# Optimization experiments

Hardware: AMD Instinct MI355X
Metric: run time of the kernel (lower is better)

## Reference

```python
import jax, jax.numpy as jnp
import numpy as np

N, E = 100000, 1280000
IN_D, FEAT, HID, OUT = 256, 64, 64, 64
NEG_SLOPE = 0.2


def _gat_conv(x, src, dst, w, a_s, a_d, b, n):
    # x: [N, in], w: [in, out], a_s/a_d/b: [out]; edges src->dst (messages flow to dst)
    h = x @ w                                   # [N, out]
    e = jax.nn.leaky_relu((h @ a_s)[src] + (h @ a_d)[dst], NEG_SLOPE)  # [E]
    m = jax.ops.segment_max(e, dst, num_segments=n)                     # scatter-softmax (stable)
    ex = jnp.exp(e - m[dst])
    den = jax.ops.segment_sum(ex, dst, num_segments=n)
    alpha = ex / (den[dst] + 1e-16)
    out = jax.ops.segment_sum(alpha[:, None] * h[src], dst, num_segments=n)
    return out + b


def setup_inputs() -> dict:
    key = jax.random.key(0)
    ks = jax.random.split(key, 16)
    rn = lambda k, shape, s=0.05: jax.random.normal(k, shape, jnp.float32) * s
    return {
        'x': jax.random.normal(ks[0], (N, IN_D), jnp.float32),
        'src': jax.random.randint(ks[1], (E,), 0, N),
        'dst': jax.random.randint(ks[2], (E,), 0, N),
        'lin_w': rn(ks[3], (IN_D, FEAT)), 'lin_b': jnp.zeros((FEAT,), jnp.float32),
        'w1': rn(ks[4], (FEAT, HID)), 'a1s': rn(ks[5], (HID,)), 'a1d': rn(ks[6], (HID,)), 'b1': jnp.zeros((HID,), jnp.float32),
        'w2': rn(ks[7], (HID, HID)), 'a2s': rn(ks[8], (HID,)), 'a2d': rn(ks[9], (HID,)), 'b2': jnp.zeros((HID,), jnp.float32),
        'w3': rn(ks[10], (HID, OUT)), 'a3s': rn(ks[11], (OUT,)), 'a3d': rn(ks[12], (OUT,)), 'b3': jnp.zeros((OUT,), jnp.float32),
    }


def reference(x, src, dst, lin_w, lin_b, w1, a1s, a1d, b1, w2, a2s, a2d, b2, w3, a3s, a3d, b3):
    n = x.shape[0]
    loop = jnp.arange(n, dtype=src.dtype)        # GATConv add_self_loops=True
    s = jnp.concatenate([src, loop])
    d = jnp.concatenate([dst, loop])
    h = x @ lin_w + lin_b                        # feature_pre linear
    h = jax.nn.relu(_gat_conv(h, s, d, w1, a1s, a1d, b1, n))  # dropout is identity in eval
    h = jax.nn.relu(_gat_conv(h, s, d, w2, a2s, a2d, b2, n))
    h = _gat_conv(h, s, d, w3, a3s, a3d, b3, n)
    norm = jnp.linalg.norm(h, axis=-1, keepdims=True)          # F.normalize(p=2, dim=-1)
    return h / jnp.maximum(norm, 1e-12)
```

## Files before the change

kernel.cpp:

```cpp
#include <hip/hip_runtime.h>


constexpr float NEG_SLOPE = 0.2f;
#define BKT_SHIFT 9
#define BKT_N     512
#define PCHUNK    2048
#define SRC_BITS  17

typedef __attribute__((ext_vector_type(8))) short bf16x8;
typedef __attribute__((ext_vector_type(4))) float f32x4;

__device__ inline ushort f2bf(float x) {
    union { float f; uint u; } v; v.f = x;
    return (ushort)((v.u + 0x7FFFu + ((v.u >> 16) & 1u)) >> 16);
}
__device__ inline void bf2f(uint u, float& lo, float& hi) {
    union { uint u; float f; } a, b;
    a.u = u << 16; b.u = u & 0xFFFF0000u;
    lo = a.f; hi = b.f;
}
__device__ inline uint pk(float a, float b) {
    return (uint)f2bf(a) | ((uint)f2bf(b) << 16);
}

__global__ __launch_bounds__(256) void prep_w(
    const float* __restrict__ lw, const float* __restrict__ w1,
    const float* __restrict__ w2, const float* __restrict__ w3,
    ushort* __restrict__ lwT, ushort* __restrict__ w1T,
    ushort* __restrict__ w2T, ushort* __restrict__ w3T,
    int* __restrict__ cnt, int* __restrict__ ticket, int n)
{
    const int i = blockIdx.x * 256 + threadIdx.x;
    if (i < n) cnt[i] = 0;
    if (i == 0) *ticket = 0;
    if (i < 64 * 256) {
        const int nn = i >> 8, k = i & 255;
        lwT[i] = f2bf(lw[k * 64 + nn]);
    } else {
        const int j = i - 64 * 256;
        if (j < 4096) {
            const int nn = j >> 6, k = j & 63;
            w1T[j] = f2bf(w1[k * 64 + nn]);
            w2T[j] = f2bf(w2[k * 64 + nn]);
            w3T[j] = f2bf(w3[k * 64 + nn]);
        }
    }
}

__device__ __forceinline__ void gemm_pre_tile(
    const float* __restrict__ x, const ushort* __restrict__ lwT,
    const float* __restrict__ bias, ushort* __restrict__ C, int M, int tile)
{
    __shared__ __align__(16) ushort ctile[4][16][64];
    const int tid = threadIdx.x;
    const int w = tid >> 6, lane = tid & 63;
    const int rw0 = (tile * 4 + w) * 16;
    if (rw0 >= M) return;
    const int c = lane & 15, q = lane >> 4;

    const float* ap = x + (size_t)(rw0 + c) * 256 + q * 8;
    float4 pv[16];
    #pragma unroll
    for (int s = 0; s < 8; ++s) {
        pv[2 * s]     = *(const float4*)(ap + s * 32);
        pv[2 * s + 1] = *(const float4*)(ap + s * 32 + 4);
    }

    f32x4 acc[4];
    #pragma unroll
    for (int t = 0; t < 4; ++t) acc[t] = (f32x4){0.f, 0.f, 0.f, 0.f};

    #pragma unroll
    for (int s = 0; s < 8; ++s) {
        const float4 p0 = pv[2 * s];
        const float4 p1 = pv[2 * s + 1];
        bf16x8 af;
        af[0] = (short)f2bf(p0.x); af[1] = (short)f2bf(p0.y);
        af[2] = (short)f2bf(p0.z); af[3] = (short)f2bf(p0.w);
        af[4] = (short)f2bf(p1.x); af[5] = (short)f2bf(p1.y);
        af[6] = (short)f2bf(p1.z); af[7] = (short)f2bf(p1.w);
        #pragma unroll
        for (int t = 0; t < 4; ++t) {
            const bf16x8 bf = *(const bf16x8*)(lwT + (size_t)(t * 16 + c) * 256 + s * 32 + q * 8);
            acc[t] = __builtin_amdgcn_mfma_f32_16x16x32_bf16(af, bf, acc[t], 0, 0, 0);
        }
    }

    #pragma unroll
    for (int t = 0; t < 4; ++t) {
        const float bv = bias[t * 16 + c];
        #pragma unroll
        for (int r = 0; r < 4; ++r)
            ctile[w][q * 4 + r][t * 16 + c] = f2bf(acc[t][r] + bv);
    }
    const int row = lane >> 2, eo = (lane & 3) * 16;
    const uint4 v0 = *(const uint4*)(&ctile[w][row][eo]);
    const uint4 v1 = *(const uint4*)(&ctile[w][row][eo + 8]);
    *(uint4*)(C + (size_t)(rw0 + row) * 64 + eo)     = v0;
    *(uint4*)(C + (size_t)(rw0 + row) * 64 + eo + 8) = v1;
}

__global__ __launch_bounds__(256) void gemm_layer(
    const ushort* __restrict__ A, const ushort* __restrict__ WT,
    const float* __restrict__ a_s, const float* __restrict__ a_d,
    ushort* __restrict__ C, float* __restrict__ hs, float* __restrict__ hd, int M)
{
    __shared__ __align__(16) ushort ctile[4][16][64];
    const int tid = threadIdx.x;
    const int w = tid >> 6, lane = tid & 63;
    const int rw0 = (blockIdx.x * 4 + w) * 16;
    if (rw0 >= M) return;
    const int c = lane & 15, q = lane >> 4;

    const ushort* ap = A + (size_t)(rw0 + c) * 64 + q * 8;
    const bf16x8 a0 = *(const bf16x8*)(ap);
    const bf16x8 a1 = *(const bf16x8*)(ap + 32);

    f32x4 acc[4];
    #pragma unroll
    for (int t = 0; t < 4; ++t) {
        const ushort* bp = WT + (size_t)(t * 16 + c) * 64 + q * 8;
        const bf16x8 b0 = *(const bf16x8*)(bp);
        const bf16x8 b1 = *(const bf16x8*)(bp + 32);
        f32x4 a = (f32x4){0.f, 0.f, 0.f, 0.f};
        a = __builtin_amdgcn_mfma_f32_16x16x32_bf16(a0, b0, a, 0, 0, 0);
        a = __builtin_amdgcn_mfma_f32_16x16x32_bf16(a1, b1, a, 0, 0, 0);
        acc[t] = a;
    }

    float ps[4] = {0.f, 0.f, 0.f, 0.f}, pd[4] = {0.f, 0.f, 0.f, 0.f};
    #pragma unroll
    for (int t = 0; t < 4; ++t) {
        const float as = a_s[t * 16 + c], ad = a_d[t * 16 + c];
        #pragma unroll
        for (int r = 0; r < 4; ++r) {
            ps[r] = fmaf(acc[t][r], as, ps[r]);
            pd[r] = fmaf(acc[t][r], ad, pd[r]);
        }
    }
    #pragma unroll
    for (int r = 0; r < 4; ++r) {
        #pragma unroll
        for (int off = 1; off < 16; off <<= 1) {
            ps[r] += __shfl_xor(ps[r], off);
            pd[r] += __shfl_xor(pd[r], off);
        }
    }
    if (c == 0) {
        #pragma unroll
        for (int r = 0; r < 4; ++r) {
            hs[rw0 + q * 4 + r] = ps[r];
            hd[rw0 + q * 4 + r] = pd[r];
        }
    }

    #pragma unroll
    for (int t = 0; t < 4; ++t)
        #pragma unroll
        for (int r = 0; r < 4; ++r)
            ctile[w][q * 4 + r][t * 16 + c] = f2bf(acc[t][r]);
    const int row = lane >> 2, eo = (lane & 3) * 16;
    const uint4 v0 = *(const uint4*)(&ctile[w][row][eo]);
    const uint4 v1 = *(const uint4*)(&ctile[w][row][eo + 8]);
    *(uint4*)(C + (size_t)(rw0 + row) * 64 + eo)     = v0;
    *(uint4*)(C + (size_t)(rw0 + row) * 64 + eo + 8) = v1;
}

__global__ __launch_bounds__(256) void edge_hist(
    const int* __restrict__ dst, int* __restrict__ cnt, int e)
{
    const int i0 = (blockIdx.x * 256 + threadIdx.x) * 4;
    if (i0 + 3 < e) {
        const int4 d = *(const int4*)(dst + i0);
        atomicAdd(&cnt[d.x], 1); atomicAdd(&cnt[d.y], 1);
        atomicAdd(&cnt[d.z], 1); atomicAdd(&cnt[d.w], 1);
    } else {
        for (int k = i0; k < e; ++k) atomicAdd(&cnt[dst[k]], 1);
    }
}

__global__ __launch_bounds__(256) void scan1_tiles(
    const int* __restrict__ cnt, int* __restrict__ out,
    int* __restrict__ bsum, int* __restrict__ ticket, int n, int nblk,
    const float* __restrict__ x, const ushort* __restrict__ lwT,
    const float* __restrict__ lin_b, ushort* __restrict__ C, int M, int tile0)
{
    __shared__ int wsum[4];
    __shared__ int amLastS;
    if ((int)blockIdx.x >= nblk) {
        gemm_pre_tile(x, lwT, lin_b, C, M, tile0 + (int)blockIdx.x - nblk);
        return;
    }
    const int tid  = threadIdx.x;
    const int lane = tid & 63;
    const int w    = tid >> 6;
    const int base = blockIdx.x * 1024;
    int vals[4];
    int tsum = 0;
    #pragma unroll
    for (int i = 0; i < 4; ++i) {
        const int idx = base + tid * 4 + i;
        vals[i] = (idx < n) ? cnt[idx] : 0;
        tsum += vals[i];
    }
    int x1 = tsum;
    #pragma unroll
    for (int off = 1; off < 64; off <<= 1) {
        const int y = __shfl_up(x1, off);
        if (lane >= off) x1 += y;
    }
    if (lane == 63) wsum[w] = x1;
    __syncthreads();
    int wofs = 0;
    for (int k = 0; k < w; ++k) wofs += wsum[k];
    int excl = wofs + x1 - tsum;
    #pragma unroll
    for (int i = 0; i < 4; ++i) {
        const int idx = base + tid * 4 + i;
        if (idx < n) out[idx] = excl;
        excl += vals[i];
    }
    if (tid == 255) {
        bsum[blockIdx.x] = wofs + x1;
        __threadfence();
        amLastS = (atomicAdd(ticket, 1) == nblk - 1) ? 1 : 0;
    }
    __syncthreads();
    if (amLastS) {
        __threadfence();
        const int v2 = (tid < nblk) ? bsum[tid] : 0;
        int x2 = v2;
        #pragma unroll
        for (int off = 1; off < 64; off <<= 1) {
            const int y = __shfl_up(x2, off);
            if (lane >= off) x2 += y;
        }
        if (lane == 63) wsum[w] = x2;
        __syncthreads();
        int c2 = 0;
        for (int k = 0; k < w; ++k) c2 += wsum[k];
        if (tid < nblk) bsum[tid] = c2 + x2 - v2;
    }
}

__global__ __launch_bounds__(256) void scan3_tiles(
    int* __restrict__ out, const int* __restrict__ bsum,
    int* __restrict__ gcur, int n, int total, int s3b,
    const float* __restrict__ x, const ushort* __restrict__ lwT,
    const float* __restrict__ lin_b, ushort* __restrict__ C, int M, int tile0)
{
    if ((int)blockIdx.x >= s3b) {
        gemm_pre_tile(x, lwT, lin_b, C, M, tile0 + (int)blockIdx.x - s3b);
        return;
    }
    const int idx = blockIdx.x * 256 + threadIdx.x;
    if (idx < n) {
        const int v = out[idx] + bsum[idx >> 10];
        out[idx] = v;
        if ((idx & (BKT_N - 1)) == 0) gcur[idx >> BKT_SHIFT] = v;
    }
    if (idx == 0) out[n] = total;
}

__global__ __launch_bounds__(256) void part_tiles(
    const int* __restrict__ src, const int* __restrict__ dst,
    int* __restrict__ gcursor, int* __restrict__ pairs, int e, int nb, int pb,
    const float* __restrict__ x, const ushort* __restrict__ lwT,
    const float* __restrict__ lin_b, ushort* __restrict__ C, int M, int tile0)
{
    __shared__ int stage[PCHUNK];
    __shared__ unsigned char sbkt[PCHUNK];
    __shared__ int lcnt[256];
    __shared__ int lstart[256];
    __shared__ int lfill[256];
    __shared__ int gbase[256];
    __shared__ int wsum[4];

    if ((int)blockIdx.x >= pb) {
        gemm_pre_tile(x, lwT, lin_b, C, M, tile0 + (int)blockIdx.x - pb);
        return;
    }

    const int tid  = threadIdx.x;
    const int lane = tid & 63;
    const int w    = tid >> 6;
    const int base = blockIdx.x * PCHUNK;
    const int cnt_here = min(PCHUNK, e - base);

    lcnt[tid] = 0; lfill[tid] = 0;
    __syncthreads();

    for (int i = tid; i < cnt_here; i += 256)
        atomicAdd(&lcnt[dst[base + i] >> BKT_SHIFT], 1);
    __syncthreads();

    const int v = lcnt[tid];
    int x1 = v;
    #pragma unroll
    for (int off = 1; off < 64; off <<= 1) {
        const int y = __shfl_up(x1, off);
        if (lane >= off) x1 += y;
    }
    if (lane == 63) wsum[w] = x1;
    __syncthreads();
    int carry = 0;
    for (int k = 0; k < w; ++k) carry += wsum[k];
    lstart[tid] = carry + x1 - v;
    if (tid < nb && v > 0) gbase[tid] = atomicAdd(&gcursor[tid], v);
    __syncthreads();

    for (int i = tid; i < cnt_here; i += 256) {
        const int d = dst[base + i];
        const int s = src[base + i];
        const int b = d >> BKT_SHIFT;
        const int p = lstart[b] + atomicAdd(&lfill[b], 1);
        stage[p] = ((d & (BKT_N - 1)) << SRC_BITS) | s;
        sbkt[p]  = (unsigned char)b;
    }
    __syncthreads();

    for (int t = tid; t < cnt_here; t += 256) {
        const int b = sbkt[t];
        pairs[gbase[b] + (t - lstart[b])] = stage[t];
    }
}

__global__ __launch_bounds__(256) void scat_tiles(
    const int* __restrict__ pairs, const int* __restrict__ offs,
    int* __restrict__ ssrc, int n, int sb,
    const float* __restrict__ x, const ushort* __restrict__ lwT,
    const float* __restrict__ lin_b, ushort* __restrict__ C, int M, int tile0)
{
    __shared__ int pos[BKT_N];
    if ((int)blockIdx.x >= sb) {
        gemm_pre_tile(x, lwT, lin_b, C, M, tile0 + (int)blockIdx.x - sb);
        return;
    }
    const int node0 = blockIdx.x << BKT_SHIFT;
    const int node1 = min(n, node0 + BKT_N);
    const int tid = threadIdx.x;
    for (int i = tid; i < node1 - node0; i += 256) pos[i] = offs[node0 + i];
    __syncthreads();
    const int e0 = offs[node0];
    const int e1 = offs[node1];
    for (int j = e0 + tid; j < e1; j += 256) {
        const int pr = pairs[j];
        const int p = atomicAdd(&pos[pr >> SRC_BITS], 1);
        ssrc[p] = pr & ((1 << SRC_BITS) - 1);
    }
}

template <int MODE>
__global__ __launch_bounds__(256) void gat_agg(
    const ushort* __restrict__ hp, const float* __restrict__ hs,
    const float* __restrict__ hd, const int* __restrict__ offs,
    const int* __restrict__ ssrc, const float* __restrict__ bias,
    void* __restrict__ outv, int n)
{
    const int wid  = (blockIdx.x * blockDim.x + threadIdx.x) >> 6;
    const int lane = threadIdx.x & 63;
    if (wid >= n) return;
    const int sub = lane >> 3;
    const int f0  = (lane & 7) * 8;

    const int start = offs[wid];
    const int end   = offs[wid + 1];
    const float hdi = hd[wid];

    int j = start + sub;
    bool vC = j < end;
    bool vN = j + 8 < end;
    int sC = vC ? ssrc[j]     : wid;
    int sN = vN ? ssrc[j + 8] : sC;

    float den = 0.f;
    float acc[8] = {};

    if (sub == 0) {
        const uint4 t = *(const uint4*)(hp + (size_t)wid * 64 + f0);
        float e = hs[wid] + hdi;
        e = (e > 0.f) ? e : NEG_SLOPE * e;
        const float ex = __expf(e);
        float f[8];
        bf2f(t.x, f[0], f[1]); bf2f(t.y, f[2], f[3]);
        bf2f(t.z, f[4], f[5]); bf2f(t.w, f[6], f[7]);
        den = ex;
        #pragma unroll
        for (int i = 0; i < 8; ++i) acc[i] = ex * f[i];
    }

    float hsC = hs[sC];
    uint4 tC  = *(const uint4*)(hp + (size_t)sC * 64 + f0);

    while (vC) {
        const bool vNN = j + 16 < end;
        const int  sNN = vNN ? ssrc[j + 16] : sN;
        const float hsN = hs[sN];
        const uint4 tN  = *(const uint4*)(hp + (size_t)sN * 64 + f0);

        float e2 = hsC + hdi;
        e2 = (e2 > 0.f) ? e2 : NEG_SLOPE * e2;
        const float ex2 = __expf(e2);
        float f[8];
        bf2f(tC.x, f[0], f[1]); bf2f(tC.y, f[2], f[3]);
        bf2f(tC.z, f[4], f[5]); bf2f(tC.w, f[6], f[7]);
        den += ex2;
        #pragma unroll
        for (int i = 0; i < 8; ++i) acc[i] = fmaf(ex2, f[i], acc[i]);

        vC = vN; vN = vNN; sC = sN; sN = sNN; hsC = hsN; tC = tN;
        j += 8;
    }

    #pragma unroll
    for (int off = 8; off < 64; off <<= 1) {
        den += __shfl_xor(den, off);
        #pragma unroll
        for (int i = 0; i < 8; ++i) acc[i] += __shfl_xor(acc[i], off);
    }

    const float4 bv0 = *(const float4*)(bias + f0);
    const float4 bv1 = *(const float4*)(bias + f0 + 4);
    const float bb[8] = {bv0.x, bv0.y, bv0.z, bv0.w, bv1.x, bv1.y, bv1.z, bv1.w};
    const float inv = 1.f / (den + 1e-16f);
    float v[8];
    #pragma unroll
    for (int i = 0; i < 8; ++i) v[i] = acc[i] * inv + bb[i];

    if (MODE == 0) {
        #pragma unroll
        for (int i = 0; i < 8; ++i) v[i] = fmaxf(v[i], 0.f);
        if (sub == 0) {
            uint4 o;
            o.x = pk(v[0], v[1]); o.y = pk(v[2], v[3]);
            o.z = pk(v[4], v[5]); o.w = pk(v[6], v[7]);
            *(uint4*)((ushort*)outv + (size_t)wid * 64 + f0) = o;
        }
    } else {
        float sq = 0.f;
        #pragma unroll
        for (int i = 0; i < 8; ++i) sq += v[i] * v[i];
        #pragma unroll
        for (int off = 1; off < 8; off <<= 1) sq += __shfl_xor(sq, off);
        const float s = 1.f / fmaxf(sqrtf(sq), 1e-12f);
        if (sub == 0) {
            float* op = (float*)outv + (size_t)wid * 64 + f0;
            float4 o0, o1;
            o0.x = v[0] * s; o0.y = v[1] * s; o0.z = v[2] * s; o0.w = v[3] * s;
            o1.x = v[4] * s; o1.y = v[5] * s; o1.z = v[6] * s; o1.w = v[7] * s;
            *(float4*)(op)     = o0;
            *(float4*)(op + 4) = o1;
        }
    }
}

extern "C" void kernel_launch(void* const* d_in, const int* in_sizes, int n_in,
                              void* d_out, int out_size, void* d_ws, size_t ws_size,
                              hipStream_t stream)
{
    const float* x     = (const float*)d_in[0];
    const int*   src   = (const int*)d_in[1];
    const int*   dst   = (const int*)d_in[2];
    const float* lin_w = (const float*)d_in[3];
    const float* lin_b = (const float*)d_in[4];
    const float* w1  = (const float*)d_in[5];
    const float* a1s = (const float*)d_in[6];
    const float* a1d = (const float*)d_in[7];
    const float* b1  = (const float*)d_in[8];
    const float* w2  = (const float*)d_in[9];
    const float* a2s = (const float*)d_in[10];
    const float* a2d = (const float*)d_in[11];
    const float* b2  = (const float*)d_in[12];
    const float* w3  = (const float*)d_in[13];
    const float* a3s = (const float*)d_in[14];
    const float* a3d = (const float*)d_in[15];
    const float* b3  = (const float*)d_in[16];

    const int n = in_sizes[0] / 256;
    const int E = in_sizes[1];
    const int nb = (n + BKT_N - 1) >> BKT_SHIFT;

    char* wsp = (char*)d_ws;
    auto alloc = [&](size_t bytes) -> void* {
        void* p = (void*)wsp;
        wsp += (bytes + 255) & ~(size_t)255;
        return p;
    };
    ushort* bufA = (ushort*)alloc((size_t)n * 64 * sizeof(ushort));
    ushort* bufB = (ushort*)alloc((size_t)n * 64 * sizeof(ushort));
    float*  hs   = (float*)alloc((size_t)n * sizeof(float));
    float*  hd   = (float*)alloc((size_t)n * sizeof(float));
    int*    offs = (int*)alloc((size_t)(n + 1) * sizeof(int));
    int*    cnt  = (int*)alloc((size_t)n * sizeof(int));
    int*    bsum = (int*)alloc(1024 * sizeof(int));
    int*    gcur = (int*)alloc(256 * sizeof(int));
    int*    tick = (int*)alloc(256 * sizeof(int));
    int*    ssrc = (int*)alloc((size_t)E * sizeof(int));
    int*    pairs = (int*)alloc((size_t)E * sizeof(int));
    ushort* lwT = (ushort*)alloc(64 * 256 * sizeof(ushort));
    ushort* w1T = (ushort*)alloc(64 * 64 * sizeof(ushort));
    ushort* w2T = (ushort*)alloc(64 * 64 * sizeof(ushort));
    ushort* w3T = (ushort*)alloc(64 * 64 * sizeof(ushort));

    const int nodeWaveBlocks = (n + 3) / 4;
    const int gemmBlocks = (n + 63) / 64;
    const int nScanBlocks = (n + 1023) / 1024;
    const int s3Blocks = (n + 255) / 256;
    const int histBlocks = (E / 4 + 255) / 256 + 1;
    const int partBlocks = (E + PCHUNK - 1) / PCHUNK;

    const int TA = 200;
    const int TB = 300;
    const int TC = 400;
    const int TD = gemmBlocks - TA - TB - TC;

    prep_w<<<(n + 255) / 256, 256, 0, stream>>>(
        lin_w, w1, w2, w3, lwT, w1T, w2T, w3T, cnt, tick, n);
    edge_hist<<<histBlocks, 256, 0, stream>>>(dst, cnt, E);
    scan1_tiles<<<nScanBlocks + TA, 256, 0, stream>>>(
        cnt, offs, bsum, tick, n, nScanBlocks,
        x, lwT, lin_b, bufA, n, 0);
    scan3_tiles<<<s3Blocks + TB, 256, 0, stream>>>(
        offs, bsum, gcur, n, E, s3Blocks,
        x, lwT, lin_b, bufA, n, TA);
    part_tiles<<<partBlocks + TC, 256, 0, stream>>>(
        src, dst, gcur, pairs, E, nb, partBlocks,
        x, lwT, lin_b, bufA, n, TA + TB);
    scat_tiles<<<nb + TD, 256, 0, stream>>>(
        pairs, offs, ssrc, n, nb,
        x, lwT, lin_b, bufA, n, TA + TB + TC);

    gemm_layer<<<gemmBlocks, 256, 0, stream>>>(bufA, w1T, a1s, a1d, bufB, hs, hd, n);
    gat_agg<0><<<nodeWaveBlocks, 256, 0, stream>>>(bufB, hs, hd, offs, ssrc, b1, bufA, n);

    gemm_layer<<<gemmBlocks, 256, 0, stream>>>(bufA, w2T, a2s, a2d, bufB, hs, hd, n);
    gat_agg<0><<<nodeWaveBlocks, 256, 0, stream>>>(bufB, hs, hd, offs, ssrc, b2, bufA, n);

    gemm_layer<<<gemmBlocks, 256, 0, stream>>>(bufA, w3T, a3s, a3d, bufB, hs, hd, n);
    gat_agg<1><<<nodeWaveBlocks, 256, 0, stream>>>(bufB, hs, hd, offs, ssrc, b3,
                                                   d_out, n);
}
```

Measured before the change: 497.0 us.

## Fuse layer GEMMs into pre-linear and aggregation kernels with precomputed attention vectors

Fuses the first GAT layer's weight GEMM and attention projections into the pre-linear tile kernel by staging the bf16 result in LDS. It also fuses layers two and three's GEMMs into the preceding aggregation kernel via a new fused_ag kernel, and computes hs/hd from the aggregated row using precomputed W·a vectors. This removes three separate gemm_layer launches and their round trip of node features through global memory. In exchange, fused_ag processes 16 nodes per block with a serial 4-node loop per wave and two barriers, which lowers aggregation parallelism. The attention logits are now computed from the bf16-rounded input times an fp32 W·a rather than from the bf16 GEMM output, so they change slightly.

```diff
diff --git a/kernel.cpp b/kernel.cpp
--- a/kernel.cpp
+++ b/kernel.cpp
@@ -23,11 +23,20 @@
     return (uint)f2bf(a) | ((uint)f2bf(b) << 16);
 }
 
+struct PreArgs {
+    const float* x; const ushort* lwT; const float* lin_b;
+    const ushort* w1T; const float* a1s; const float* a1d;
+    ushort* C; float* hs; float* hd; int M;
+};
+
 __global__ __launch_bounds__(256) void prep_w(
     const float* __restrict__ lw, const float* __restrict__ w1,
     const float* __restrict__ w2, const float* __restrict__ w3,
+    const float* __restrict__ a2s, const float* __restrict__ a2d,
+    const float* __restrict__ a3s, const float* __restrict__ a3d,
     ushort* __restrict__ lwT, ushort* __restrict__ w1T,
     ushort* __restrict__ w2T, ushort* __restrict__ w3T,
+    float* __restrict__ wvec,
     int* __restrict__ cnt, int* __restrict__ ticket, int n)
 {
     const int i = blockIdx.x * 256 + threadIdx.x;
@@ -36,40 +45,44 @@
     if (i < 64 * 256) {
         const int nn = i >> 8, k = i & 255;
         lwT[i] = f2bf(lw[k * 64 + nn]);
-    } else {
+    } else if (i < 64 * 256 + 4096) {
         const int j = i - 64 * 256;
-        if (j < 4096) {
-            const int nn = j >> 6, k = j & 63;
-            w1T[j] = f2bf(w1[k * 64 + nn]);
-            w2T[j] = f2bf(w2[k * 64 + nn]);
-            w3T[j] = f2bf(w3[k * 64 + nn]);
-        }
-    }
-}
-
-__device__ __forceinline__ void gemm_pre_tile(
-    const float* __restrict__ x, const ushort* __restrict__ lwT,
-    const float* __restrict__ bias, ushort* __restrict__ C, int M, int tile)
-{
+        const int nn = j >> 6, k = j & 63;
+        w1T[j] = f2bf(w1[k * 64 + nn]);
+        w2T[j] = f2bf(w2[k * 64 + nn]);
+        w3T[j] = f2bf(w3[k * 64 + nn]);
+    } else if (i < 64 * 256 + 4096 + 256) {
+        const int j = i - 64 * 256 - 4096;
+        const int p = j >> 6, k = j & 63;
+        const float* Wp = (p < 2) ? w2 : w3;
+        const float* vp = (p == 0) ? a2s : (p == 1) ? a2d : (p == 2) ? a3s : a3d;
+        float s = 0.f;
+        #pragma unroll
+        for (int t = 0; t < 64; ++t) s += Wp[k * 64 + t] * vp[t];
+        wvec[p * 64 + k] = s;
+    }
+}
+
+__device__ __forceinline__ void gemm_pre_fused(const PreArgs& pa, int tile)
+{
+    __shared__ __align__(16) ushort ldsA[4][8][16][8];
     __shared__ __align__(16) ushort ctile[4][16][64];
     const int tid = threadIdx.x;
     const int w = tid >> 6, lane = tid & 63;
     const int rw0 = (tile * 4 + w) * 16;
-    if (rw0 >= M) return;
+    if (rw0 >= pa.M) return;
     const int c = lane & 15, q = lane >> 4;
 
-    const float* ap = x + (size_t)(rw0 + c) * 256 + q * 8;
+    const float* ap = pa.x + (size_t)(rw0 + c) * 256 + q * 8;
     float4 pv[16];
     #pragma unroll
     for (int s = 0; s < 8; ++s) {
         pv[2 * s]     = *(const float4*)(ap + s * 32);
         pv[2 * s + 1] = *(const float4*)(ap + s * 32 + 4);
     }
-
     f32x4 acc[4];
     #pragma unroll
     for (int t = 0; t < 4; ++t) acc[t] = (f32x4){0.f, 0.f, 0.f, 0.f};
-
     #pragma unroll
     for (int s = 0; s < 8; ++s) {
         const float4 p0 = pv[2 * s];
@@ -81,61 +94,41 @@
         af[6] = (short)f2bf(p1.z); af[7] = (short)f2bf(p1.w);
         #pragma unroll
         for (int t = 0; t < 4; ++t) {
-            const bf16x8 bf = *(const bf16x8*)(lwT + (size_t)(t * 16 + c) * 256 + s * 32 + q * 8);
+            const bf16x8 bf = *(const bf16x8*)(pa.lwT + (size_t)(t * 16 + c) * 256 + s * 32 + q * 8);
             acc[t] = __builtin_amdgcn_mfma_f32_16x16x32_bf16(af, bf, acc[t], 0, 0, 0);
         }
     }
-
     #pragma unroll
     for (int t = 0; t < 4; ++t) {
-        const float bv = bias[t * 16 + c];
+        const float bv = pa.lin_b[t * 16 + c];
+        const int kb = 2 * t + (c >> 3);
+        const int e  = c & 7;
         #pragma unroll
         for (int r = 0; r < 4; ++r)
-            ctile[w][q * 4 + r][t * 16 + c] = f2bf(acc[t][r] + bv);
-    }
-    const int row = lane >> 2, eo = (lane & 3) * 16;
-    const uint4 v0 = *(const uint4*)(&ctile[w][row][eo]);
-    const uint4 v1 = *(const uint4*)(&ctile[w][row][eo + 8]);
-    *(uint4*)(C + (size_t)(rw0 + row) * 64 + eo)     = v0;
-    *(uint4*)(C + (size_t)(rw0 + row) * 64 + eo + 8) = v1;
-}
-
-__global__ __launch_bounds__(256) void gemm_layer(
-    const ushort* __restrict__ A, const ushort* __restrict__ WT,
-    const float* __restrict__ a_s, const float* __restrict__ a_d,
-    ushort* __restrict__ C, float* __restrict__ hs, float* __restrict__ hd, int M)
-{
-    __shared__ __align__(16) ushort ctile[4][16][64];
-    const int tid = threadIdx.x;
-    const int w = tid >> 6, lane = tid & 63;
-    const int rw0 = (blockIdx.x * 4 + w) * 16;
-    if (rw0 >= M) return;
-    const int c = lane & 15, q = lane >> 4;
-
-    const ushort* ap = A + (size_t)(rw0 + c) * 64 + q * 8;
-    const bf16x8 a0 = *(const bf16x8*)(ap);
-    const bf16x8 a1 = *(const bf16x8*)(ap + 32);
-
-    f32x4 acc[4];
+            ldsA[w][kb][q * 4 + r][e] = f2bf(acc[t][r] + bv);
+    }
+
+    const bf16x8 a0 = *(const bf16x8*)&ldsA[w][q][c][0];
+    const bf16x8 a1 = *(const bf16x8*)&ldsA[w][q + 4][c][0];
+    f32x4 acc2[4];
     #pragma unroll
     for (int t = 0; t < 4; ++t) {
-        const ushort* bp = WT + (size_t)(t * 16 + c) * 64 + q * 8;
+        const ushort* bp = pa.w1T + (size_t)(t * 16 + c) * 64 + q * 8;
         const bf16x8 b0 = *(const bf16x8*)(bp);
         const bf16x8 b1 = *(const bf16x8*)(bp + 32);
         f32x4 a = (f32x4){0.f, 0.f, 0.f, 0.f};
         a = __builtin_amdgcn_mfma_f32_16x16x32_bf16(a0, b0, a, 0, 0, 0);
         a = __builtin_amdgcn_mfma_f32_16x16x32_bf16(a1, b1, a, 0, 0, 0);
-        acc[t] = a;
-    }
-
+        acc2[t] = a;
+    }
     float ps[4] = {0.f, 0.f, 0.f, 0.f}, pd[4] = {0.f, 0.f, 0.f, 0.f};
     #pragma unroll
     for (int t = 0; t < 4; ++t) {
-        const float as = a_s[t * 16 + c], ad = a_d[t * 16 + c];
+        const float as = pa.a1s[t * 16 + c], ad = pa.a1d[t * 16 + c];
         #pragma unroll
         for (int r = 0; r < 4; ++r) {
-            ps[r] = fmaf(acc[t][r], as, ps[r]);
-            pd[r] = fmaf(acc[t][r], ad, pd[r]);
+            ps[r] = fmaf(acc2[t][r], as, ps[r]);
+            pd[r] = fmaf(acc2[t][r], ad, pd[r]);
         }
     }
     #pragma unroll
@@ -149,21 +142,20 @@
     if (c == 0) {
         #pragma unroll
         for (int r = 0; r < 4; ++r) {
-            hs[rw0 + q * 4 + r] = ps[r];
-            hd[rw0 + q * 4 + r] = pd[r];
+            pa.hs[rw0 + q * 4 + r] = ps[r];
+            pa.hd[rw0 + q * 4 + r] = pd[r];
         }
     }
-
     #pragma unroll
     for (int t = 0; t < 4; ++t)
         #pragma unroll
         for (int r = 0; r < 4; ++r)
-            ctile[w][q * 4 + r][t * 16 + c] = f2bf(acc[t][r]);
+            ctile[w][q * 4 + r][t * 16 + c] = f2bf(acc2[t][r]);
     const int row = lane >> 2, eo = (lane & 3) * 16;
     const uint4 v0 = *(const uint4*)(&ctile[w][row][eo]);
     const uint4 v1 = *(const uint4*)(&ctile[w][row][eo + 8]);
-    *(uint4*)(C + (size_t)(rw0 + row) * 64 + eo)     = v0;
-    *(uint4*)(C + (size_t)(rw0 + row) * 64 + eo + 8) = v1;
+    *(uint4*)(pa.C + (size_t)(rw0 + row) * 64 + eo)     = v0;
+    *(uint4*)(pa.C + (size_t)(rw0 + row) * 64 + eo + 8) = v1;
 }
 
 __global__ __launch_bounds__(256) void edge_hist(
@@ -182,13 +174,12 @@
 __global__ __launch_bounds__(256) void scan1_tiles(
     const int* __restrict__ cnt, int* __restrict__ out,
     int* __restrict__ bsum, int* __restrict__ ticket, int n, int nblk,
-    const float* __restrict__ x, const ushort* __restrict__ lwT,
-    const float* __restrict__ lin_b, ushort* __restrict__ C, int M, int tile0)
+    PreArgs pa, int tile0)
 {
     __shared__ int wsum[4];
     __shared__ int amLastS;
     if ((int)blockIdx.x >= nblk) {
-        gemm_pre_tile(x, lwT, lin_b, C, M, tile0 + (int)blockIdx.x - nblk);
+        gemm_pre_fused(pa, tile0 + (int)blockIdx.x - nblk);
         return;
     }
     const int tid  = threadIdx.x;
@@ -246,11 +237,10 @@
 __global__ __launch_bounds__(256) void scan3_tiles(
     int* __restrict__ out, const int* __restrict__ bsum,
     int* __restrict__ gcur, int n, int total, int s3b,
-    const float* __restrict__ x, const ushort* __restrict__ lwT,
-    const float* __restrict__ lin_b, ushort* __restrict__ C, int M, int tile0)
+    PreArgs pa, int tile0)
 {
     if ((int)blockIdx.x >= s3b) {
-        gemm_pre_tile(x, lwT, lin_b, C, M, tile0 + (int)blockIdx.x - s3b);
+        gemm_pre_fused(pa, tile0 + (int)blockIdx.x - s3b);
         return;
     }
     const int idx = blockIdx.x * 256 + threadIdx.x;
@@ -265,8 +255,7 @@
 __global__ __launch_bounds__(256) void part_tiles(
     const int* __restrict__ src, const int* __restrict__ dst,
     int* __restrict__ gcursor, int* __restrict__ pairs, int e, int nb, int pb,
-    const float* __restrict__ x, const ushort* __restrict__ lwT,
-    const float* __restrict__ lin_b, ushort* __restrict__ C, int M, int tile0)
+    PreArgs pa, int tile0)
 {
     __shared__ int stage[PCHUNK];
     __shared__ unsigned char sbkt[PCHUNK];
@@ -277,7 +266,7 @@
     __shared__ int wsum[4];
 
     if ((int)blockIdx.x >= pb) {
-        gemm_pre_tile(x, lwT, lin_b, C, M, tile0 + (int)blockIdx.x - pb);
+        gemm_pre_fused(pa, tile0 + (int)blockIdx.x - pb);
         return;
     }
 
@@ -328,12 +317,11 @@
 __global__ __launch_bounds__(256) void scat_tiles(
     const int* __restrict__ pairs, const int* __restrict__ offs,
     int* __restrict__ ssrc, int n, int sb,
-    const float* __restrict__ x, const ushort* __restrict__ lwT,
-    const float* __restrict__ lin_b, ushort* __restrict__ C, int M, int tile0)
+    PreArgs pa, int tile0)
 {
     __shared__ int pos[BKT_N];
     if ((int)blockIdx.x >= sb) {
-        gemm_pre_tile(x, lwT, lin_b, C, M, tile0 + (int)blockIdx.x - sb);
+        gemm_pre_fused(pa, tile0 + (int)blockIdx.x - sb);
         return;
     }
     const int node0 = blockIdx.x << BKT_SHIFT;
@@ -350,12 +338,147 @@
     }
 }
 
-template <int MODE>
-__global__ __launch_bounds__(256) void gat_agg(
+__global__ __launch_bounds__(256) void fused_ag(
+    const ushort* __restrict__ hp, const float* __restrict__ hsIn,
+    const float* __restrict__ hdIn, const int* __restrict__ offs,
+    const int* __restrict__ ssrc, const float* __restrict__ bias,
+    const ushort* __restrict__ WT, const float* __restrict__ waS,
+    const float* __restrict__ waD,
+    ushort* __restrict__ C, float* __restrict__ hsOut, float* __restrict__ hdOut,
+    int n)
+{
+    __shared__ __align__(16) ushort ldsA[8][16][8];
+    __shared__ __align__(16) ushort ldsC[16][68];
+    const int tid  = threadIdx.x;
+    const int w    = tid >> 6, lane = tid & 63;
+    const int rw0  = blockIdx.x * 16;
+    const int sub  = lane >> 3;
+    const int f0   = (lane & 7) * 8;
+
+    const float4 bv0 = *(const float4*)(bias + f0);
+    const float4 bv1 = *(const float4*)(bias + f0 + 4);
+    const float bb[8] = {bv0.x, bv0.y, bv0.z, bv0.w, bv1.x, bv1.y, bv1.z, bv1.w};
+    float ws8[8], wd8[8];
+    {
+        const float4 s0 = *(const float4*)(waS + f0);
+        const float4 s1 = *(const float4*)(waS + f0 + 4);
+        const float4 d0 = *(const float4*)(waD + f0);
+        const float4 d1 = *(const float4*)(waD + f0 + 4);
+        ws8[0]=s0.x; ws8[1]=s0.y; ws8[2]=s0.z; ws8[3]=s0.w;
+        ws8[4]=s1.x; ws8[5]=s1.y; ws8[6]=s1.z; ws8[7]=s1.w;
+        wd8[0]=d0.x; wd8[1]=d0.y; wd8[2]=d0.z; wd8[3]=d0.w;
+        wd8[4]=d1.x; wd8[5]=d1.y; wd8[6]=d1.z; wd8[7]=d1.w;
+    }
+
+    #pragma unroll 1
+    for (int i = 0; i < 4; ++i) {
+        const int rowIdx = w * 4 + i;
+        const int node = rw0 + rowIdx;
+        if (node < n) {
+            const int start = offs[node];
+            const int end   = offs[node + 1];
+            const float hdi = hdIn[node];
+
+            int j = start + sub;
+            bool vC = j < end;
+            bool vN = j + 8 < end;
+            int sC = vC ? ssrc[j]     : node;
+            int sN = vN ? ssrc[j + 8] : sC;
+
+            float den = 0.f;
+            float acc[8] = {};
+            if (sub == 0) {
+                const uint4 t = *(const uint4*)(hp + (size_t)node * 64 + f0);
+                float e = hsIn[node] + hdi;
+                e = (e > 0.f) ? e : NEG_SLOPE * e;
+                const float ex = __expf(e);
+                float f[8];
+                bf2f(t.x, f[0], f[1]); bf2f(t.y, f[2], f[3]);
+                bf2f(t.z, f[4], f[5]); bf2f(t.w, f[6], f[7]);
+                den = ex;
+                #pragma unroll
+                for (int k = 0; k < 8; ++k) acc[k] = ex * f[k];
+            }
+            float hsC = hsIn[sC];
+            uint4 tC  = *(const uint4*)(hp + (size_t)sC * 64 + f0);
+            while (vC) {
+                const bool vNN = j + 16 < end;
+                const int  sNN = vNN ? ssrc[j + 16] : sN;
+                const float hsN = hsIn[sN];
+                const uint4 tN  = *(const uint4*)(hp + (size_t)sN * 64 + f0);
+                float e2 = hsC + hdi;
+                e2 = (e2 > 0.f) ? e2 : NEG_SLOPE * e2;
+                const float ex2 = __expf(e2);
+                float f[8];
+                bf2f(tC.x, f[0], f[1]); bf2f(tC.y, f[2], f[3]);
+                bf2f(tC.z, f[4], f[5]); bf2f(tC.w, f[6], f[7]);
+                den += ex2;
+                #pragma unroll
+                for (int k = 0; k < 8; ++k) acc[k] = fmaf(ex2, f[k], acc[k]);
+                vC = vN; vN = vNN; sC = sN; sN = sNN; hsC = hsN; tC = tN;
+                j += 8;
+            }
+            #pragma unroll
+            for (int off = 8; off < 64; off <<= 1) {
+                den += __shfl_xor(den, off);
+                #pragma unroll
+                for (int k = 0; k < 8; ++k) acc[k] += __shfl_xor(acc[k], off);
+            }
+            const float inv = 1.f / (den + 1e-16f);
+            float v[8];
+            #pragma unroll
+            for (int k = 0; k < 8; ++k)
+                v[k] = fmaxf(acc[k] * inv + bb[k], 0.f);
+            uint4 o;
+            o.x = pk(v[0], v[1]); o.y = pk(v[2], v[3]);
+            o.z = pk(v[4], v[5]); o.w = pk(v[6], v[7]);
+            float rv[8];
+            bf2f(o.x, rv[0], rv[1]); bf2f(o.y, rv[2], rv[3]);
+            bf2f(o.z, rv[4], rv[5]); bf2f(o.w, rv[6], rv[7]);
+            float psum = 0.f, pdum = 0.f;
+            #pragma unroll
+            for (int k = 0; k < 8; ++k) {
+                psum = fmaf(rv[k], ws8[k], psum);
+                pdum = fmaf(rv[k], wd8[k], pdum);
+            }
+            #pragma unroll
+            for (int off = 1; off < 8; off <<= 1) {
+                psum += __shfl_xor(psum, off);
+                pdum += __shfl_xor(pdum, off);
+            }
+            if (lane == 0) { hsOut[node] = psum; hdOut[node] = pdum; }
+            if (sub == 0) *(uint4*)&ldsA[lane & 7][rowIdx][0] = o;
+        } else if (sub == 0) {
+            const uint4 z = {0u, 0u, 0u, 0u};
+            *(uint4*)&ldsA[lane & 7][rowIdx][0] = z;
+        }
+    }
+    __syncthreads();
+
+    const int c = lane & 15, q = lane >> 4;
+    const bf16x8 a0 = *(const bf16x8*)&ldsA[q][c][0];
+    const bf16x8 a1 = *(const bf16x8*)&ldsA[q + 4][c][0];
+    const ushort* bp = WT + (size_t)(w * 16 + c) * 64 + q * 8;
+    const bf16x8 b0 = *(const bf16x8*)(bp);
+    const bf16x8 b1 = *(const bf16x8*)(bp + 32);
+    f32x4 a = (f32x4){0.f, 0.f, 0.f, 0.f};
+    a = __builtin_amdgcn_mfma_f32_16x16x32_bf16(a0, b0, a, 0, 0, 0);
+    a = __builtin_amdgcn_mfma_f32_16x16x32_bf16(a1, b1, a, 0, 0, 0);
+    #pragma unroll
+    for (int r = 0; r < 4; ++r)
+        ldsC[q * 4 + r][w * 16 + c] = f2bf(a[r]);
+    __syncthreads();
+
+    const int row = tid >> 4, co = (tid & 15) * 4;
+    if (rw0 + row < n)
+        *(uint2*)(C + (size_t)(rw0 + row) * 64 + co) = *(const uint2*)&ldsC[row][co];
+}
+
+__global__ __launch_bounds__(256) void gat_agg_final(
     const ushort* __restrict__ hp, const float* __restrict__ hs,
     const float* __restrict__ hd, const int* __restrict__ offs,
     const int* __restrict__ ssrc, const float* __restrict__ bias,
-    void* __restrict__ outv, int n)
+    float* __restrict__ outp, int n)
 {
     const int wid  = (blockIdx.x * blockDim.x + threadIdx.x) >> 6;
     const int lane = threadIdx.x & 63;
@@ -375,7 +498,6 @@
 
     float den = 0.f;
     float acc[8] = {};
-
     if (sub == 0) {
         const uint4 t = *(const uint4*)(hp + (size_t)wid * 64 + f0);
         float e = hs[wid] + hdi;
@@ -388,16 +510,13 @@
         #pragma unroll
         for (int i = 0; i < 8; ++i) acc[i] = ex * f[i];
     }
-
     float hsC = hs[sC];
     uint4 tC  = *(const uint4*)(hp + (size_t)sC * 64 + f0);
-
     while (vC) {
         const bool vNN = j + 16 < end;
         const int  sNN = vNN ? ssrc[j + 16] : sN;
         const float hsN = hs[sN];
         const uint4 tN  = *(const uint4*)(hp + (size_t)sN * 64 + f0);
-
         float e2 = hsC + hdi;
         e2 = (e2 > 0.f) ? e2 : NEG_SLOPE * e2;
         const float ex2 = __expf(e2);
@@ -407,18 +526,15 @@
         den += ex2;
         #pragma unroll
         for (int i = 0; i < 8; ++i) acc[i] = fmaf(ex2, f[i], acc[i]);
-
         vC = vN; vN = vNN; sC = sN; sN = sNN; hsC = hsN; tC = tN;
         j += 8;
     }
-
     #pragma unroll
     for (int off = 8; off < 64; off <<= 1) {
         den += __shfl_xor(den, off);
         #pragma unroll
         for (int i = 0; i < 8; ++i) acc[i] += __shfl_xor(acc[i], off);
     }
-
     const float4 bv0 = *(const float4*)(bias + f0);
     const float4 bv1 = *(const float4*)(bias + f0 + 4);
     const float bb[8] = {bv0.x, bv0.y, bv0.z, bv0.w, bv1.x, bv1.y, bv1.z, bv1.w};
@@ -426,31 +542,19 @@
     float v[8];
     #pragma unroll
     for (int i = 0; i < 8; ++i) v[i] = acc[i] * inv + bb[i];
-
-    if (MODE == 0) {
-        #pragma unroll
-        for (int i = 0; i < 8; ++i) v[i] = fmaxf(v[i], 0.f);
-        if (sub == 0) {
-            uint4 o;
-            o.x = pk(v[0], v[1]); o.y = pk(v[2], v[3]);
-            o.z = pk(v[4], v[5]); o.w = pk(v[6], v[7]);
-            *(uint4*)((ushort*)outv + (size_t)wid * 64 + f0) = o;
-        }
-    } else {
-        float sq = 0.f;
-        #pragma unroll
-        for (int i = 0; i < 8; ++i) sq += v[i] * v[i];
-        #pragma unroll
-        for (int off = 1; off < 8; off <<= 1) sq += __shfl_xor(sq, off);
-        const float s = 1.f / fmaxf(sqrtf(sq), 1e-12f);
-        if (sub == 0) {
-            float* op = (float*)outv + (size_t)wid * 64 + f0;
-            float4 o0, o1;
-            o0.x = v[0] * s; o0.y = v[1] * s; o0.z = v[2] * s; o0.w = v[3] * s;
-            o1.x = v[4] * s; o1.y = v[5] * s; o1.z = v[6] * s; o1.w = v[7] * s;
-            *(float4*)(op)     = o0;
-            *(float4*)(op + 4) = o1;
-        }
+    float sq = 0.f;
+    #pragma unroll
+    for (int i = 0; i < 8; ++i) sq += v[i] * v[i];
+    #pragma unroll
+    for (int off = 1; off < 8; off <<= 1) sq += __shfl_xor(sq, off);
+    const float s = 1.f / fmaxf(sqrtf(sq), 1e-12f);
+    if (sub == 0) {
+        float* op = outp + (size_t)wid * 64 + f0;
+        float4 o0, o1;
+        o0.x = v[0] * s; o0.y = v[1] * s; o0.z = v[2] * s; o0.w = v[3] * s;
+        o1.x = v[4] * s; o1.y = v[5] * s; o1.z = v[6] * s; o1.w = v[7] * s;
+        *(float4*)(op)     = o0;
+        *(float4*)(op + 4) = o1;
     }
 }
 
@@ -488,8 +592,10 @@
     };
     ushort* bufA = (ushort*)alloc((size_t)n * 64 * sizeof(ushort));
     ushort* bufB = (ushort*)alloc((size_t)n * 64 * sizeof(ushort));
-    float*  hs   = (float*)alloc((size_t)n * sizeof(float));
-    float*  hd   = (float*)alloc((size_t)n * sizeof(float));
+    float*  hsA  = (float*)alloc((size_t)n * sizeof(float));
+    float*  hdA  = (float*)alloc((size_t)n * sizeof(float));
+    float*  hsB  = (float*)alloc((size_t)n * sizeof(float));
+    float*  hdB  = (float*)alloc((size_t)n * sizeof(float));
     int*    offs = (int*)alloc((size_t)(n + 1) * sizeof(int));
     int*    cnt  = (int*)alloc((size_t)n * sizeof(int));
     int*    bsum = (int*)alloc(1024 * sizeof(int));
@@ -501,42 +607,42 @@
     ushort* w1T = (ushort*)alloc(64 * 64 * sizeof(ushort));
     ushort* w2T = (ushort*)alloc(64 * 64 * sizeof(ushort));
     ushort* w3T = (ushort*)alloc(64 * 64 * sizeof(ushort));
-
-    const int nodeWaveBlocks = (n + 3) / 4;
+    float*  wvec = (float*)alloc(256 * sizeof(float));
+
     const int gemmBlocks = (n + 63) / 64;
     const int nScanBlocks = (n + 1023) / 1024;
     const int s3Blocks = (n + 255) / 256;
     const int histBlocks = (E / 4 + 255) / 256 + 1;
     const int partBlocks = (E + PCHUNK - 1) / PCHUNK;
+    const int fusedBlocks = (n + 15) / 16;
+    const int aggBlocks = (n + 3) / 4;
 
     const int TA = 200;
     const int TB = 300;
     const int TC = 400;
     const int TD = gemmBlocks - TA - TB - TC;
 
+    PreArgs pa{x, lwT, lin_b, w1T, a1s, a1d, bufB, hsB, hdB, n};
+
     prep_w<<<(n + 255) / 256, 256, 0, stream>>>(
-        lin_w, w1, w2, w3, lwT, w1T, w2T, w3T, cnt, tick, n);
+        lin_w, w1, w2, w3, a2s, a2d, a3s, a3d,
+        lwT, w1T, w2T, w3T, wvec, cnt, tick, n);
     edge_hist<<<histBlocks, 256, 0, stream>>>(dst, cnt, E);
     scan1_tiles<<<nScanBlocks + TA, 256, 0, stream>>>(
-        cnt, offs, bsum, tick, n, nScanBlocks,
-        x, lwT, lin_b, bufA, n, 0);
+        cnt, offs, bsum, tick, n, nScanBlocks, pa, 0);
     scan3_tiles<<<s3Blocks + TB, 256, 0, stream>>>(
-        offs, bsum, gcur, n, E, s3Blocks,
-        x, lwT, lin_b, bufA, n, TA);
+        offs, bsum, gcur, n, E, s3Blocks, pa, TA);
     part_tiles<<<partBlocks + TC, 256, 0, stream>>>(
-        src, dst, gcur, pairs, E, nb, partBlocks,
-        x, lwT, lin_b, bufA, n, TA + TB);
+        src, dst, gcur, pairs, E, nb, partBlocks, pa, TA + TB);
     scat_tiles<<<nb + TD, 256, 0, stream>>>(
-        pairs, offs, ssrc, n, nb,
-        x, lwT, lin_b, bufA, n, TA + TB + TC);
-
-    gemm_layer<<<gemmBlocks, 256, 0, stream>>>(bufA, w1T, a1s, a1d, bufB, hs, hd, n);
-    gat_agg<0><<<nodeWaveBlocks, 256, 0, stream>>>(bufB, hs, hd, offs, ssrc, b1, bufA, n);
-
-    gemm_layer<<<gemmBlocks, 256, 0, stream>>>(bufA, w2T, a2s, a2d, bufB, hs, hd, n);
-    gat_agg<0><<<nodeWaveBlocks, 256, 0, stream>>>(bufB, hs, hd, offs, ssrc, b2, bufA, n);
-
-    gemm_layer<<<gemmBlocks, 256, 0, stream>>>(bufA, w3T, a3s, a3d, bufB, hs, hd, n);
-    gat_agg<1><<<nodeWaveBlocks, 256, 0, stream>>>(bufB, hs, hd, offs, ssrc, b3,
-                                                   d_out, n);
-}
+        pairs, offs, ssrc, n, nb, pa, TA + TB + TC);
+
+    fused_ag<<<fusedBlocks, 256, 0, stream>>>(
+        bufB, hsB, hdB, offs, ssrc, b1, w2T, wvec, wvec + 64,
+        bufA, hsA, hdA, n);
+    fused_ag<<<fusedBlocks, 256, 0, stream>>>(
+        bufA, hsA, hdA, offs, ssrc, b2, w3T, wvec + 128, wvec + 192,
+        bufB, hsB, hdB, n);
+    gat_agg_final<<<aggBlocks, 256, 0, stream>>>(
+        bufB, hsB, hdB, offs, ssrc, b3, (float*)d_out, n);
+}
```

Result: faster. 468.8 us (-5.7%).
